# Performance work log

Hardware: AMD Instinct MI355X
Metric: run time of the kernel (lower is better)

The kernel has to match this reference:

```python
import jax, jax.numpy as jnp
import numpy as np

B, T, C, H = 2, 2048, 1024, 16
HD = C // H  # 64
EPS = 1e-5


def _layernorm(x, g, b):
    mu = jnp.mean(x, axis=-1, keepdims=True)
    var = jnp.mean(jnp.square(x - mu), axis=-1, keepdims=True)
    return (x - mu) * jax.lax.rsqrt(var + EPS) * g + b


def setup_inputs() -> dict:
    key = jax.random.key(0)
    ks = jax.random.split(key, 12)
    s = 0.02
    return {
        "x": jax.random.normal(ks[0], (B, T, C), dtype=jnp.float32),
        # per-head q/k/v projections stacked over heads: [H, C, HD]
        "Wq": jax.random.normal(ks[1], (H, C, HD), dtype=jnp.float32) * s,
        "Wk": jax.random.normal(ks[2], (H, C, HD), dtype=jnp.float32) * s,
        "Wv": jax.random.normal(ks[3], (H, C, HD), dtype=jnp.float32) * s,
        "Wp": jax.random.normal(ks[4], (C, C), dtype=jnp.float32) * s,
        "bp": jnp.zeros((C,), dtype=jnp.float32),
        "W1": jax.random.normal(ks[5], (C, 4 * C), dtype=jnp.float32) * s,
        "b1": jnp.zeros((4 * C,), dtype=jnp.float32),
        "W2": jax.random.normal(ks[6], (4 * C, C), dtype=jnp.float32) * s,
        "b2": jnp.zeros((C,), dtype=jnp.float32),
        "g1": jnp.ones((C,), dtype=jnp.float32),
        "be1": jnp.zeros((C,), dtype=jnp.float32),
        "g2": jnp.ones((C,), dtype=jnp.float32),
        "be2": jnp.zeros((C,), dtype=jnp.float32),
    }


def reference(x, Wq, Wk, Wv, Wp, bp, W1, b1, W2, b2, g1, be1, g2, be2):
    b, t, c = x.shape
    hd = Wq.shape[-1]
    # multi-head causal self-attention (heads vectorized instead of Python loop)
    q = jnp.einsum('btc,hcd->bhtd', x, Wq)
    k = jnp.einsum('btc,hcd->bhtd', x, Wk)
    v = jnp.einsum('btc,hcd->bhtd', x, Wv)
    scores = jnp.einsum('bhtd,bhsd->bhts', q, k) * (float(hd) ** -0.5)
    causal = jnp.tril(jnp.ones((t, t), dtype=bool))
    scores = jnp.where(causal, scores, -jnp.inf)
    probs = jax.nn.softmax(scores, axis=-1)  # dropout is identity in eval
    o = jnp.einsum('bhts,bhsd->bhtd', probs, v)
    o = o.transpose(0, 2, 1, 3).reshape(b, t, c)  # concat heads
    attn_out = o @ Wp + bp
    # residual + post-norm
    x = _layernorm(x + attn_out, g1, be1)
    # FFN (dropout identity in eval)
    ff = jax.nn.relu(x @ W1 + b1) @ W2 + b2
    x = _layernorm(x + ff, g2, be2)
    return x
```

## Files before the change

kernel.cpp:

```cpp
#include <hip/hip_runtime.h>
#include <cstdint>
#include <cstddef>

typedef __attribute__((ext_vector_type(8))) short short8;
typedef __attribute__((ext_vector_type(4))) short short4v;
typedef __attribute__((ext_vector_type(4))) float f32x4;
typedef __attribute__((ext_vector_type(2))) uint32_t u32x2;

#define Bdim 2
#define Tdim 2048
#define Cdim 1024
#define Hdim 16
#define HDdim 64
#define Mdim (Bdim*Tdim)
#define FFdim (4*Cdim)

__device__ __forceinline__ uint16_t f2bf(float f) {
    union { float f; uint32_t u; } v; v.f = f;
    uint32_t x = v.u;
    uint32_t r = x + 0x7FFFu + ((x >> 16) & 1u);
    return (uint16_t)(r >> 16);
}
__device__ __forceinline__ float bf2f(uint16_t h) {
    union { float f; uint32_t u; } v; v.u = ((uint32_t)h) << 16; return v.f;
}
__device__ __forceinline__ uint32_t cvtpk(float lo, float hi) {
    uint32_t r;
    asm("v_cvt_pk_bf16_f32 %0, %1, %2" : "=v"(r) : "v"(lo), "v"(hi));
    return r;
}

__device__ __forceinline__ void gload_lds16(const uint16_t* g, uint16_t* l) {
    __builtin_amdgcn_global_load_lds(
        (const __attribute__((address_space(1))) void*)g,
        (__attribute__((address_space(3))) void*)l, 16, 0, 0);
}

#define RAW_BAR()   asm volatile("s_barrier" ::: "memory")
#define VMCNT(N)    asm volatile("s_waitcnt vmcnt(" #N ")" ::: "memory")
#define LGKM0()     asm volatile("s_waitcnt lgkmcnt(0)" ::: "memory")

__global__ __launch_bounds__(256) void cast4_k(const float* __restrict__ in,
                                               uint16_t* __restrict__ out) {
    int i = (blockIdx.x * 256 + threadIdx.x) * 4;
    f32x4 v = *(const f32x4*)(in + i);
    short4v o;
#pragma unroll
    for (int j = 0; j < 4; ++j) o[j] = (short)f2bf(v[j]);
    *(short4v*)(out + i) = o;
}

__global__ __launch_bounds__(256) void transpose_tile(const float* __restrict__ in,
                                                      uint16_t* __restrict__ out,
                                                      int R, int Cc,
                                                      size_t ibs, size_t obs) {
    __shared__ uint16_t tile[32][33];
    const float* ip = in + (size_t)blockIdx.z * ibs;
    uint16_t* op = out + (size_t)blockIdx.z * obs;
    int r0 = blockIdx.x * 32, n0 = blockIdx.y * 32;
    int tx = threadIdx.x, ty = threadIdx.y;
#pragma unroll
    for (int i = 0; i < 4; ++i) {
        int r = ty + 8 * i;
        tile[r][tx] = f2bf(ip[(size_t)(r0 + r) * Cc + n0 + tx]);
    }
    __syncthreads();
#pragma unroll
    for (int i = 0; i < 4; ++i) {
        int n = ty + 8 * i;
        op[(size_t)(n0 + n) * R + r0 + tx] = tile[tx][n];
    }
}

__global__ __launch_bounds__(256) void vtrans_k(const uint16_t* __restrict__ qkv,
                                                uint16_t* __restrict__ vT) {
    __shared__ uint16_t tile[32][33];
    const int bh = blockIdx.z, b = bh >> 4, h = bh & 15;
    const uint16_t* vp = qkv + (size_t)b * Tdim * (3 * Cdim) + 2 * Cdim + h * HDdim;
    uint16_t* op = vT + (size_t)bh * HDdim * Tdim;
    const int t0 = blockIdx.x * 32, d0 = blockIdx.y * 32;
    const int tx = threadIdx.x, ty = threadIdx.y;
#pragma unroll
    for (int i = 0; i < 4; ++i) {
        int r = ty + 8 * i;
        tile[r][tx] = vp[(size_t)(t0 + r) * (3 * Cdim) + d0 + tx];
    }
    __syncthreads();
    const int tp = t0 + (((tx >> 2) & 3) << 3) + (((tx >> 4) & 1) << 2) + (tx & 3);
#pragma unroll
    for (int i = 0; i < 4; ++i) {
        int d = ty + 8 * i;
        op[(size_t)(d0 + d) * Tdim + tp] = tile[tx][d];
    }
}

template<bool BIAS, bool RELU, bool RESID, bool OUTF>
__global__ __launch_bounds__(512, 4) void gemm128_k(const uint16_t* __restrict__ A,
                                                    const uint16_t* __restrict__ Bt,
                                                    int Kfull, int Kp,
                                                    float* outF,
                                                    uint16_t* __restrict__ outB,
                                                    const float* __restrict__ bias,
                                                    const float* resid,
                                                    uint16_t* __restrict__ outP1,
                                                    uint16_t* __restrict__ outP2,
                                                    uint16_t* __restrict__ outP3,
                                                    int N) {
    __shared__ uint16_t lds[32768];
    const int bx = blockIdx.x, by = blockIdx.y, kz = blockIdx.z;
    const int tid = threadIdx.x;
    const int wave = tid >> 6, lane = tid & 63;
    const int lg = lane >> 4, lr = lane & 15, lr7 = lr & 7;
    const int wm = wave >> 2, wn = wave & 3;
    const int NT = Kp >> 6;

    const int aOff = wm * 4096 + lr * 64;
    const int bOff = 16384 + wn * 2048 + lr * 64;
    const int g0 = 8 * (lg ^ lr7);
    const int g1 = 8 * ((4 + lg) ^ lr7);

    const int srow = tid >> 3;
    const int scol = 8 * ((tid & 7) ^ (srow & 7));
    const uint16_t* aSrc = A + (size_t)(bx * 128 + srow) * Kfull + (size_t)kz * Kp + scol;
    const uint16_t* bSrc = Bt + (size_t)(by * 128 + srow) * Kfull + (size_t)kz * Kp + scol;
    const size_t r64 = (size_t)64 * Kfull;

#define STG_A(pp, tt) do {                                                        \
        _Pragma("unroll")                                                         \
        for (int h_ = 0; h_ < 2; ++h_)                                            \
            gload_lds16(aSrc + h_ * r64 + (size_t)(tt) * 64,                      \
                        &lds[(pp) * 8192 + h_ * 4096 + wave * 512]);              \
    } while (0)
#define STG_B(pp, tt) do {                                                        \
        _Pragma("unroll")                                                         \
        for (int h_ = 0; h_ < 2; ++h_)                                            \
            gload_lds16(bSrc + h_ * r64 + (size_t)(tt) * 64,                      \
                        &lds[16384 + (pp) * 8192 + h_ * 4096 + wave * 512]);      \
    } while (0)
#define MM(M, Nn, AF, BF) acc[M][Nn] = __builtin_amdgcn_mfma_f32_16x16x32_bf16(AF, BF, acc[M][Nn], 0, 0, 0)

    f32x4 acc[4][2];
#pragma unroll
    for (int i = 0; i < 4; ++i)
#pragma unroll
        for (int j = 0; j < 2; ++j) acc[i][j] = (f32x4){0.f, 0.f, 0.f, 0.f};

    STG_B(0, 0); STG_A(0, 0);
    if (NT > 1) { STG_B(1, 1); STG_A(1, 1); VMCNT(4); }
    else VMCNT(0);
    RAW_BAR();

    for (int t = 0; t < NT; ++t) {
        const int p = t & 1, p13 = p << 13;
        const bool nx1 = (t + 1 < NT), nx2 = (t + 2 < NT);
        short8 a0[4], b0[2], a1[4], b1[2];

#pragma unroll
        for (int m = 0; m < 4; ++m) a0[m] = *(const short8*)&lds[p13 + aOff + 1024 * m + g0];
#pragma unroll
        for (int nn = 0; nn < 2; ++nn) b0[nn] = *(const short8*)&lds[p13 + bOff + 1024 * nn + g0];
        __builtin_amdgcn_s_setprio(1);
#pragma unroll
        for (int m = 0; m < 4; ++m)
#pragma unroll
            for (int nn = 0; nn < 2; ++nn) MM(m, nn, a0[m], b0[nn]);
        __builtin_amdgcn_s_setprio(0);

#pragma unroll
        for (int m = 0; m < 4; ++m) a1[m] = *(const short8*)&lds[p13 + aOff + 1024 * m + g1];
#pragma unroll
        for (int nn = 0; nn < 2; ++nn) b1[nn] = *(const short8*)&lds[p13 + bOff + 1024 * nn + g1];
        __builtin_amdgcn_s_setprio(1);
#pragma unroll
        for (int m = 0; m < 4; ++m)
#pragma unroll
            for (int nn = 0; nn < 2; ++nn) MM(m, nn, a1[m], b1[nn]);
        __builtin_amdgcn_s_setprio(0);

        LGKM0();
        RAW_BAR();
        if (nx2) { STG_B(p, t + 2); STG_A(p, t + 2); }
        if (nx1) {
            if (nx2) VMCNT(4); else VMCNT(0);
            RAW_BAR();
        }
    }
#undef STG_A
#undef STG_B
#undef MM
    if (kz == 0) {
#pragma unroll
        for (int nn = 0; nn < 2; ++nn) {
            const int col = (by << 7) + wn * 32 + 16 * nn + lr;
            const float bv = BIAS ? bias[col] : 0.f;
#pragma unroll
            for (int m = 0; m < 4; ++m) {
#pragma unroll
                for (int r = 0; r < 4; ++r) {
                    const int row = (bx << 7) + wm * 64 + 16 * m + 4 * lg + r;
                    float v = acc[m][nn][r] + bv;
                    if (RELU) v = fmaxf(v, 0.f);
                    if (RESID) v += resid[(size_t)row * N + col];
                    if (OUTF) outF[(size_t)row * N + col] = v;
                    else      outB[(size_t)row * N + col] = f2bf(v);
                }
            }
        }
    } else {
        uint16_t* op = (kz == 1) ? outP1 : (kz == 2) ? outP2 : outP3;
#pragma unroll
        for (int nn = 0; nn < 2; ++nn) {
            const int col = (by << 7) + wn * 32 + 16 * nn + lr;
#pragma unroll
            for (int m = 0; m < 4; ++m) {
#pragma unroll
                for (int r = 0; r < 4; ++r) {
                    const int row = (bx << 7) + wm * 64 + 16 * m + 4 * lg + r;
                    op[(size_t)row * N + col] = f2bf(acc[m][nn][r]);
                }
            }
        }
    }
}

__global__ __launch_bounds__(256) void attn_k(const uint16_t* __restrict__ qkv,
                                              const uint16_t* __restrict__ vT,
                                              uint16_t* __restrict__ o) {
    __shared__ uint16_t Kb[2][64 * 64];
    __shared__ uint16_t Vb[2][64 * 64];
    const int tid = threadIdx.x;
    const int wave = tid >> 6, lane = tid & 63;
    const int lg = lane >> 4, lr = lane & 15, lr7 = lr & 7;
    const int bh = blockIdx.x, b = bh >> 4, h = bh & 15;
    const size_t rs = 3 * Cdim;
    const uint16_t* qp = qkv + (size_t)b * Tdim * rs + (size_t)h * HDdim;
    const uint16_t* kp = qp + Cdim;
    const uint16_t* vtp = vT + (size_t)bh * HDdim * Tdim;

    const int s0 = tid, s1 = tid + 256;
    const int r0v = s0 >> 3, c0v = ((s0 & 7) ^ (r0v & 7)) << 3;
    const int r1v = s1 >> 3, c1v = ((s1 & 7) ^ (r1v & 7)) << 3;
    const int db0 = wave * 512, db1 = 2048 + wave * 512;

#define STAGE(bufi, kvb)                                                        \
    do {                                                                        \
        gload_lds16(kp + (size_t)((kvb) + r0v) * rs + c0v, &Kb[bufi][db0]);     \
        gload_lds16(kp + (size_t)((kvb) + r1v) * rs + c1v, &Kb[bufi][db1]);     \
        gload_lds16(vtp + (size_t)r0v * Tdim + (kvb) + c0v, &Vb[bufi][db0]);    \
        gload_lds16(vtp + (size_t)r1v * Tdim + (kvb) + c1v, &Vb[bufi][db1]);    \
    } while (0)

    const int tiles[2] = {(int)blockIdx.y, 31 - (int)blockIdx.y};

    for (int ti = 0; ti < 2; ++ti) {
        const int tx = tiles[ti];
        const int q0 = tx << 6;
        const int nch = tx + 1;
        const int qrow = q0 + 16 * wave + lr;

        short8 qf[2];
#pragma unroll
        for (int c = 0; c < 2; ++c) {
            short8 raw = *(const short8*)(qp + (size_t)qrow * rs + 32 * c + 8 * lg);
#pragma unroll
            for (int j = 0; j < 8; ++j)
                qf[c][j] = (short)f2bf(bf2f((uint16_t)raw[j]) * 0.125f);
        }

        float m_run = -__builtin_inff(), l_run = 0.f;
        f32x4 oacc[4];
#pragma unroll
        for (int t = 0; t < 4; ++t) oacc[t] = (f32x4){0.f, 0.f, 0.f, 0.f};

        STAGE(0, 0);
        __syncthreads();
        int cur = 0;
        for (int ch = 0; ch < nch; ++ch) {
            if (ch + 1 < nch) STAGE(cur ^ 1, 64 * (ch + 1));
            const int kvb = 64 * ch;
            const char* Kc = (const char*)&Kb[cur][0];
            const char* Vc = (const char*)&Vb[cur][0];
            short8 kf[4][2];
#pragma unroll
            for (int u = 0; u < 4; ++u)
#pragma unroll
                for (int c = 0; c < 2; ++c)
                    kf[u][c] = *(const short8*)(Kc + (16 * u + lr) * 128 +
                                                (((lg + 4 * c) ^ lr7) << 4));
            f32x4 s4[4];
            __builtin_amdgcn_s_setprio(1);
#pragma unroll
            for (int u = 0; u < 4; ++u) {
                f32x4 z = (f32x4){0.f, 0.f, 0.f, 0.f};
                z = __builtin_amdgcn_mfma_f32_16x16x32_bf16(kf[u][0], qf[0], z, 0, 0, 0);
                z = __builtin_amdgcn_mfma_f32_16x16x32_bf16(kf[u][1], qf[1], z, 0, 0, 0);
                s4[u] = z;
            }
            __builtin_amdgcn_s_setprio(0);
            float p[4][4];
            float mx;
            if (ch + 1 == nch) {
                mx = -__builtin_inff();
#pragma unroll
                for (int u = 0; u < 4; ++u)
#pragma unroll
                    for (int r = 0; r < 4; ++r) {
                        int kv = kvb + 16 * u + 4 * lg + r;
                        float sv = (kv <= qrow) ? s4[u][r] : -__builtin_inff();
                        p[u][r] = sv;
                        mx = fmaxf(mx, sv);
                    }
            } else {
#pragma unroll
                for (int u = 0; u < 4; ++u)
#pragma unroll
                    for (int r = 0; r < 4; ++r) p[u][r] = s4[u][r];
                f32x4 m4;
#pragma unroll
                for (int r = 0; r < 4; ++r)
                    m4[r] = fmaxf(fmaxf(s4[0][r], s4[1][r]), fmaxf(s4[2][r], s4[3][r]));
                mx = fmaxf(fmaxf(m4[0], m4[1]), fmaxf(m4[2], m4[3]));
            }
            mx = fmaxf(mx, __shfl_xor(mx, 16));
            mx = fmaxf(mx, __shfl_xor(mx, 32));
            if (!__all(mx <= m_run + 8.f)) {
                const float m_new = fmaxf(m_run, mx);
                const float alpha = __expf(m_run - m_new);
#pragma unroll
                for (int t = 0; t < 4; ++t)
#pragma unroll
                    for (int r = 0; r < 4; ++r) oacc[t][r] *= alpha;
                l_run *= alpha;
                m_run = m_new;
            }
            float ps = 0.f;
#pragma unroll
            for (int u = 0; u < 4; ++u)
#pragma unroll
                for (int r = 0; r < 4; ++r) {
                    float e = __expf(p[u][r] - m_run);
                    p[u][r] = e; ps += e;
                }
            ps += __shfl_xor(ps, 16);
            ps += __shfl_xor(ps, 32);
            l_run += ps;
            short8 pb[2];
#pragma unroll
            for (int hh = 0; hh < 2; ++hh) {
                union { uint32_t w[4]; short8 v; } q_;
                q_.w[0] = cvtpk(p[2 * hh][0], p[2 * hh][1]);
                q_.w[1] = cvtpk(p[2 * hh][2], p[2 * hh][3]);
                q_.w[2] = cvtpk(p[2 * hh + 1][0], p[2 * hh + 1][1]);
                q_.w[3] = cvtpk(p[2 * hh + 1][2], p[2 * hh + 1][3]);
                pb[hh] = q_.v;
            }
            __builtin_amdgcn_s_setprio(1);
#pragma unroll
            for (int t = 0; t < 4; ++t) {
                const int vbase = (16 * t + lr) * 128;
                f32x4 oa = oacc[t];
#pragma unroll
                for (int hh = 0; hh < 2; ++hh) {
                    short8 vf = *(const short8*)(Vc + vbase + (((4 * hh + lg) ^ lr7) << 4));
                    oa = __builtin_amdgcn_mfma_f32_16x16x32_bf16(vf, pb[hh], oa, 0, 0, 0);
                }
                oacc[t] = oa;
            }
            __builtin_amdgcn_s_setprio(0);
            __syncthreads();
            cur ^= 1;
        }
        const float inv = 1.f / l_run;
        uint16_t* orow = o + (size_t)(b * Tdim + qrow) * Cdim + h * HDdim;
#pragma unroll
        for (int t = 0; t < 4; ++t) {
            u32x2 wv;
            wv[0] = cvtpk(oacc[t][0] * inv, oacc[t][1] * inv);
            wv[1] = cvtpk(oacc[t][2] * inv, oacc[t][3] * inv);
            *(u32x2*)(orow + 16 * t + 4 * lg) = wv;
        }
        __syncthreads();
    }
#undef STAGE
}

__global__ __launch_bounds__(256) void ln_k(const float* __restrict__ in,
                                            const uint16_t* __restrict__ in2b,
                                            const float* __restrict__ g,
                                            const float* __restrict__ be,
                                            float* __restrict__ outF,
                                            uint16_t* __restrict__ outB) {
    const int row = blockIdx.x, tid = threadIdx.x;
    const size_t base = (size_t)row * Cdim + tid * 4;
    f32x4 xv = *(const f32x4*)(in + base);
    if (in2b) {
        short4v yv = *(const short4v*)(in2b + base);
#pragma unroll
        for (int j = 0; j < 4; ++j) xv[j] += bf2f((uint16_t)yv[j]);
    }
    float s = xv[0] + xv[1] + xv[2] + xv[3];
    float q = xv[0] * xv[0] + xv[1] * xv[1] + xv[2] * xv[2] + xv[3] * xv[3];
#pragma unroll
    for (int off = 1; off < 64; off <<= 1) { s += __shfl_xor(s, off); q += __shfl_xor(q, off); }
    __shared__ float sm[4], sq[4];
    if ((tid & 63) == 0) { sm[tid >> 6] = s; sq[tid >> 6] = q; }
    __syncthreads();
    s = sm[0] + sm[1] + sm[2] + sm[3];
    q = sq[0] + sq[1] + sq[2] + sq[3];
    const float mu = s * (1.f / 1024.f);
    const float var = q * (1.f / 1024.f) - mu * mu;
    const float rstd = rsqrtf(var + 1e-5f);
#pragma unroll
    for (int j = 0; j < 4; ++j) {
        int col = tid * 4 + j;
        float y = (xv[j] - mu) * rstd * g[col] + be[col];
        if (outF) outF[(size_t)row * Cdim + col] = y;
        if (outB) outB[(size_t)row * Cdim + col] = f2bf(y);
    }
}

__global__ __launch_bounds__(256) void lnp_k(const float* __restrict__ in,
                                             const uint16_t* __restrict__ p2,
                                             const uint16_t* __restrict__ p3,
                                             const uint16_t* __restrict__ p4,
                                             const float* __restrict__ g,
                                             const float* __restrict__ be,
                                             float* __restrict__ outF) {
    const int row = blockIdx.x, tid = threadIdx.x;
    const size_t base = (size_t)row * Cdim + tid * 4;
    f32x4 xv = *(const f32x4*)(in + base);
    short4v a2 = *(const short4v*)(p2 + base);
    short4v a3 = *(const short4v*)(p3 + base);
    short4v a4 = *(const short4v*)(p4 + base);
#pragma unroll
    for (int j = 0; j < 4; ++j)
        xv[j] += bf2f((uint16_t)a2[j]) + bf2f((uint16_t)a3[j]) + bf2f((uint16_t)a4[j]);
    float s = xv[0] + xv[1] + xv[2] + xv[3];
    float q = xv[0] * xv[0] + xv[1] * xv[1] + xv[2] * xv[2] + xv[3] * xv[3];
#pragma unroll
    for (int off = 1; off < 64; off <<= 1) { s += __shfl_xor(s, off); q += __shfl_xor(q, off); }
    __shared__ float sm[4], sq[4];
    if ((tid & 63) == 0) { sm[tid >> 6] = s; sq[tid >> 6] = q; }
    __syncthreads();
    s = sm[0] + sm[1] + sm[2] + sm[3];
    q = sq[0] + sq[1] + sq[2] + sq[3];
    const float mu = s * (1.f / 1024.f);
    const float var = q * (1.f / 1024.f) - mu * mu;
    const float rstd = rsqrtf(var + 1e-5f);
#pragma unroll
    for (int j = 0; j < 4; ++j) {
        int col = tid * 4 + j;
        outF[(size_t)row * Cdim + col] = (xv[j] - mu) * rstd * g[col] + be[col];
    }
}

extern "C" void kernel_launch(void* const* d_in, const int* in_sizes, int n_in,
                              void* d_out, int out_size, void* d_ws, size_t ws_size,
                              hipStream_t stream) {
    const float* x   = (const float*)d_in[0];
    const float* Wq  = (const float*)d_in[1];
    const float* Wk  = (const float*)d_in[2];
    const float* Wv  = (const float*)d_in[3];
    const float* Wp  = (const float*)d_in[4];
    const float* bp  = (const float*)d_in[5];
    const float* W1  = (const float*)d_in[6];
    const float* b1  = (const float*)d_in[7];
    const float* W2  = (const float*)d_in[8];
    const float* b2  = (const float*)d_in[9];
    const float* g1  = (const float*)d_in[10];
    const float* be1 = (const float*)d_in[11];
    const float* g2  = (const float*)d_in[12];
    const float* be2 = (const float*)d_in[13];
    float* out = (float*)d_out;

    char* ws = (char*)d_ws;
    uint16_t* qkv   = (uint16_t*)(ws + 0);
    uint16_t* P1p   = (uint16_t*)(ws + 0);
    uint16_t* h1    = (uint16_t*)(ws + 0);
    uint16_t* obuf  = (uint16_t*)(ws + 25165824);
    uint16_t* xb    = (uint16_t*)(ws + 33554432);
    uint16_t* vT    = (uint16_t*)(ws + 33554432);
    uint16_t* x1b   = (uint16_t*)(ws + 33554432);
    uint16_t* Q2    = (uint16_t*)(ws + 33554432);
    uint16_t* wqkv  = (uint16_t*)(ws + 41943040);
    uint16_t* wpt   = (uint16_t*)(ws + 48234496);
    float*    resid = (float*)   (ws + 50331648);
    uint16_t* Q1    = (uint16_t*)(ws + 50331648);
    float*    x1f   = (float*)   (ws + 67108864);
    uint16_t* w1t   = (uint16_t*)(ws + 83886080);
    uint16_t* w2t   = (uint16_t*)(ws + 92274688);
    uint16_t* Q3    = (uint16_t*)(ws + 100663296);

    cast4_k<<<4096, 256, 0, stream>>>(x, xb);
    transpose_tile<<<dim3(32, 2, 16), dim3(32, 8), 0, stream>>>(Wq, wqkv,           1024, 64, 65536, 65536);
    transpose_tile<<<dim3(32, 2, 16), dim3(32, 8), 0, stream>>>(Wk, wqkv + 1048576, 1024, 64, 65536, 65536);
    transpose_tile<<<dim3(32, 2, 16), dim3(32, 8), 0, stream>>>(Wv, wqkv + 2097152, 1024, 64, 65536, 65536);
    transpose_tile<<<dim3(32, 32, 1),  dim3(32, 8), 0, stream>>>(Wp, wpt, 1024, 1024, 0, 0);
    transpose_tile<<<dim3(32, 128, 1), dim3(32, 8), 0, stream>>>(W1, w1t, 1024, 4096, 0, 0);
    transpose_tile<<<dim3(128, 32, 1), dim3(32, 8), 0, stream>>>(W2, w2t, 4096, 1024, 0, 0);

    gemm128_k<false, false, false, false><<<dim3(32, 24, 1), 512, 0, stream>>>(
        xb, wqkv, Cdim, Cdim, nullptr, qkv, nullptr, nullptr,
        nullptr, nullptr, nullptr, 3 * Cdim);
    vtrans_k<<<dim3(64, 2, 32), dim3(32, 8), 0, stream>>>(qkv, vT);
    attn_k<<<dim3(32, 16), 256, 0, stream>>>(qkv, vT, obuf);
    gemm128_k<true, false, true, true><<<dim3(32, 8, 2), 512, 0, stream>>>(
        obuf, wpt, Cdim, Cdim / 2, resid, nullptr, bp, x,
        P1p, nullptr, nullptr, Cdim);
    ln_k<<<Mdim, 256, 0, stream>>>(resid, P1p, g1, be1, x1f, x1b);
    gemm128_k<true, true, false, false><<<dim3(32, 32, 1), 512, 0, stream>>>(
        x1b, w1t, Cdim, Cdim, nullptr, h1, b1, nullptr,
        nullptr, nullptr, nullptr, FFdim);
    gemm128_k<true, false, true, true><<<dim3(32, 8, 4), 512, 0, stream>>>(
        h1, w2t, FFdim, FFdim / 4, x1f, nullptr, b2, x1f,
        Q1, Q2, Q3, Cdim);
    lnp_k<<<Mdim, 256, 0, stream>>>(x1f, Q1, Q2, Q3, g2, be2, out);
}
```

Baseline: 244.5 us.

## Split attention into one query tile per block with exp2 softmax and lane-local sums

The attention kernel now runs one query tile per block on a 32x32 grid, instead of each block processing a paired short/long tile. Tiles are ordered in interleaved groups so heavy and light causal tiles mix across the grid. The softmax folds log2(e) into the Q scale so it can use exp2f, and it keeps row sums per lane, reducing them across lanes once at the end. The max reduction is skipped when no lane exceeds the threshold, which is raised to 11.5 in the log2 domain. This doubles the block count and removes per-chunk shuffles, at the cost of relying on the hardware scheduler for load balance.

```diff
diff --git a/kernel.cpp b/kernel.cpp
--- a/kernel.cpp
+++ b/kernel.cpp
@@ -232,6 +232,8 @@
     const int wave = tid >> 6, lane = tid & 63;
     const int lg = lane >> 4, lr = lane & 15, lr7 = lr & 7;
     const int bh = blockIdx.x, b = bh >> 4, h = bh & 15;
+    const int yy = blockIdx.y, k4 = yy >> 3, y0 = yy & 7;
+    const int tx = (k4 == 0) ? y0 : (k4 == 1) ? 31 - y0 : (k4 == 2) ? 8 + y0 : 23 - y0;
     const size_t rs = 3 * Cdim;
     const uint16_t* qp = qkv + (size_t)b * Tdim * rs + (size_t)h * HDdim;
     const uint16_t* kp = qp + Cdim;
@@ -250,136 +252,129 @@
         gload_lds16(vtp + (size_t)r1v * Tdim + (kvb) + c1v, &Vb[bufi][db1]);    \
     } while (0)
 
-    const int tiles[2] = {(int)blockIdx.y, 31 - (int)blockIdx.y};
-
-    for (int ti = 0; ti < 2; ++ti) {
-        const int tx = tiles[ti];
-        const int q0 = tx << 6;
-        const int nch = tx + 1;
-        const int qrow = q0 + 16 * wave + lr;
-
-        short8 qf[2];
-#pragma unroll
-        for (int c = 0; c < 2; ++c) {
-            short8 raw = *(const short8*)(qp + (size_t)qrow * rs + 32 * c + 8 * lg);
-#pragma unroll
-            for (int j = 0; j < 8; ++j)
-                qf[c][j] = (short)f2bf(bf2f((uint16_t)raw[j]) * 0.125f);
-        }
-
-        float m_run = -__builtin_inff(), l_run = 0.f;
-        f32x4 oacc[4];
-#pragma unroll
-        for (int t = 0; t < 4; ++t) oacc[t] = (f32x4){0.f, 0.f, 0.f, 0.f};
-
-        STAGE(0, 0);
+    const int q0 = tx << 6;
+    const int nch = tx + 1;
+    const int qrow = q0 + 16 * wave + lr;
+
+    short8 qf[2];
+#pragma unroll
+    for (int c = 0; c < 2; ++c) {
+        short8 raw = *(const short8*)(qp + (size_t)qrow * rs + 32 * c + 8 * lg);
+#pragma unroll
+        for (int j = 0; j < 8; ++j)
+            qf[c][j] = (short)f2bf(bf2f((uint16_t)raw[j]) * 0.18033688f);
+    }
+
+    float m_run = -__builtin_inff(), l_lane = 0.f;
+    f32x4 oacc[4];
+#pragma unroll
+    for (int t = 0; t < 4; ++t) oacc[t] = (f32x4){0.f, 0.f, 0.f, 0.f};
+
+    STAGE(0, 0);
+    __syncthreads();
+    int cur = 0;
+    for (int ch = 0; ch < nch; ++ch) {
+        if (ch + 1 < nch) STAGE(cur ^ 1, 64 * (ch + 1));
+        const int kvb = 64 * ch;
+        const char* Kc = (const char*)&Kb[cur][0];
+        const char* Vc = (const char*)&Vb[cur][0];
+        short8 kf[4][2];
+#pragma unroll
+        for (int u = 0; u < 4; ++u)
+#pragma unroll
+            for (int c = 0; c < 2; ++c)
+                kf[u][c] = *(const short8*)(Kc + (16 * u + lr) * 128 +
+                                            (((lg + 4 * c) ^ lr7) << 4));
+        f32x4 s4[4];
+        __builtin_amdgcn_s_setprio(1);
+#pragma unroll
+        for (int u = 0; u < 4; ++u) {
+            f32x4 z = (f32x4){0.f, 0.f, 0.f, 0.f};
+            z = __builtin_amdgcn_mfma_f32_16x16x32_bf16(kf[u][0], qf[0], z, 0, 0, 0);
+            z = __builtin_amdgcn_mfma_f32_16x16x32_bf16(kf[u][1], qf[1], z, 0, 0, 0);
+            s4[u] = z;
+        }
+        __builtin_amdgcn_s_setprio(0);
+        float p[4][4];
+        float mxl;
+        if (ch + 1 == nch) {
+            mxl = -__builtin_inff();
+#pragma unroll
+            for (int u = 0; u < 4; ++u)
+#pragma unroll
+                for (int r = 0; r < 4; ++r) {
+                    int kv = kvb + 16 * u + 4 * lg + r;
+                    float sv = (kv <= qrow) ? s4[u][r] : -__builtin_inff();
+                    p[u][r] = sv;
+                    mxl = fmaxf(mxl, sv);
+                }
+        } else {
+#pragma unroll
+            for (int u = 0; u < 4; ++u)
+#pragma unroll
+                for (int r = 0; r < 4; ++r) p[u][r] = s4[u][r];
+            f32x4 m4;
+#pragma unroll
+            for (int r = 0; r < 4; ++r)
+                m4[r] = fmaxf(fmaxf(s4[0][r], s4[1][r]), fmaxf(s4[2][r], s4[3][r]));
+            mxl = fmaxf(fmaxf(m4[0], m4[1]), fmaxf(m4[2], m4[3]));
+        }
+        if (!__all(mxl <= m_run + 11.5f)) {
+            float mx = fmaxf(mxl, __shfl_xor(mxl, 16));
+            mx = fmaxf(mx, __shfl_xor(mx, 32));
+            const float m_new = fmaxf(m_run, mx);
+            const float alpha = exp2f(m_run - m_new);
+#pragma unroll
+            for (int t = 0; t < 4; ++t)
+#pragma unroll
+                for (int r = 0; r < 4; ++r) oacc[t][r] *= alpha;
+            l_lane *= alpha;
+            m_run = m_new;
+        }
+#pragma unroll
+        for (int u = 0; u < 4; ++u)
+#pragma unroll
+            for (int r = 0; r < 4; ++r) {
+                float e = exp2f(p[u][r] - m_run);
+                p[u][r] = e; l_lane += e;
+            }
+        short8 pb[2];
+#pragma unroll
+        for (int hh = 0; hh < 2; ++hh) {
+            union { uint32_t w[4]; short8 v; } q_;
+            q_.w[0] = cvtpk(p[2 * hh][0], p[2 * hh][1]);
+            q_.w[1] = cvtpk(p[2 * hh][2], p[2 * hh][3]);
+            q_.w[2] = cvtpk(p[2 * hh + 1][0], p[2 * hh + 1][1]);
+            q_.w[3] = cvtpk(p[2 * hh + 1][2], p[2 * hh + 1][3]);
+            pb[hh] = q_.v;
+        }
+        __builtin_amdgcn_s_setprio(1);
+#pragma unroll
+        for (int t = 0; t < 4; ++t) {
+            const int vbase = (16 * t + lr) * 128;
+            f32x4 oa = oacc[t];
+#pragma unroll
+            for (int hh = 0; hh < 2; ++hh) {
+                short8 vf = *(const short8*)(Vc + vbase + (((4 * hh + lg) ^ lr7) << 4));
+                oa = __builtin_amdgcn_mfma_f32_16x16x32_bf16(vf, pb[hh], oa, 0, 0, 0);
+            }
+            oacc[t] = oa;
+        }
+        __builtin_amdgcn_s_setprio(0);
         __syncthreads();
-        int cur = 0;
-        for (int ch = 0; ch < nch; ++ch) {
-            if (ch + 1 < nch) STAGE(cur ^ 1, 64 * (ch + 1));
-            const int kvb = 64 * ch;
-            const char* Kc = (const char*)&Kb[cur][0];
-            const char* Vc = (const char*)&Vb[cur][0];
-            short8 kf[4][2];
-#pragma unroll
-            for (int u = 0; u < 4; ++u)
-#pragma unroll
-                for (int c = 0; c < 2; ++c)
-                    kf[u][c] = *(const short8*)(Kc + (16 * u + lr) * 128 +
-                                                (((lg + 4 * c) ^ lr7) << 4));
-            f32x4 s4[4];
-            __builtin_amdgcn_s_setprio(1);
-#pragma unroll
-            for (int u = 0; u < 4; ++u) {
-                f32x4 z = (f32x4){0.f, 0.f, 0.f, 0.f};
-                z = __builtin_amdgcn_mfma_f32_16x16x32_bf16(kf[u][0], qf[0], z, 0, 0, 0);
-                z = __builtin_amdgcn_mfma_f32_16x16x32_bf16(kf[u][1], qf[1], z, 0, 0, 0);
-                s4[u] = z;
-            }
-            __builtin_amdgcn_s_setprio(0);
-            float p[4][4];
-            float mx;
-            if (ch + 1 == nch) {
-                mx = -__builtin_inff();
-#pragma unroll
-                for (int u = 0; u < 4; ++u)
-#pragma unroll
-                    for (int r = 0; r < 4; ++r) {
-                        int kv = kvb + 16 * u + 4 * lg + r;
-                        float sv = (kv <= qrow) ? s4[u][r] : -__builtin_inff();
-                        p[u][r] = sv;
-                        mx = fmaxf(mx, sv);
-                    }
-            } else {
-#pragma unroll
-                for (int u = 0; u < 4; ++u)
-#pragma unroll
-                    for (int r = 0; r < 4; ++r) p[u][r] = s4[u][r];
-                f32x4 m4;
-#pragma unroll
-                for (int r = 0; r < 4; ++r)
-                    m4[r] = fmaxf(fmaxf(s4[0][r], s4[1][r]), fmaxf(s4[2][r], s4[3][r]));
-                mx = fmaxf(fmaxf(m4[0], m4[1]), fmaxf(m4[2], m4[3]));
-            }
-            mx = fmaxf(mx, __shfl_xor(mx, 16));
-            mx = fmaxf(mx, __shfl_xor(mx, 32));
-            if (!__all(mx <= m_run + 8.f)) {
-                const float m_new = fmaxf(m_run, mx);
-                const float alpha = __expf(m_run - m_new);
-#pragma unroll
-                for (int t = 0; t < 4; ++t)
-#pragma unroll
-                    for (int r = 0; r < 4; ++r) oacc[t][r] *= alpha;
-                l_run *= alpha;
-                m_run = m_new;
-            }
-            float ps = 0.f;
-#pragma unroll
-            for (int u = 0; u < 4; ++u)
-#pragma unroll
-                for (int r = 0; r < 4; ++r) {
-                    float e = __expf(p[u][r] - m_run);
-                    p[u][r] = e; ps += e;
-                }
-            ps += __shfl_xor(ps, 16);
-            ps += __shfl_xor(ps, 32);
-            l_run += ps;
-            short8 pb[2];
-#pragma unroll
-            for (int hh = 0; hh < 2; ++hh) {
-                union { uint32_t w[4]; short8 v; } q_;
-                q_.w[0] = cvtpk(p[2 * hh][0], p[2 * hh][1]);
-                q_.w[1] = cvtpk(p[2 * hh][2], p[2 * hh][3]);
-                q_.w[2] = cvtpk(p[2 * hh + 1][0], p[2 * hh + 1][1]);
-                q_.w[3] = cvtpk(p[2 * hh + 1][2], p[2 * hh + 1][3]);
-                pb[hh] = q_.v;
-            }
-            __builtin_amdgcn_s_setprio(1);
-#pragma unroll
-            for (int t = 0; t < 4; ++t) {
-                const int vbase = (16 * t + lr) * 128;
-                f32x4 oa = oacc[t];
-#pragma unroll
-                for (int hh = 0; hh < 2; ++hh) {
-                    short8 vf = *(const short8*)(Vc + vbase + (((4 * hh + lg) ^ lr7) << 4));
-                    oa = __builtin_amdgcn_mfma_f32_16x16x32_bf16(vf, pb[hh], oa, 0, 0, 0);
-                }
-                oacc[t] = oa;
-            }
-            __builtin_amdgcn_s_setprio(0);
-            __syncthreads();
-            cur ^= 1;
-        }
-        const float inv = 1.f / l_run;
-        uint16_t* orow = o + (size_t)(b * Tdim + qrow) * Cdim + h * HDdim;
-#pragma unroll
-        for (int t = 0; t < 4; ++t) {
-            u32x2 wv;
-            wv[0] = cvtpk(oacc[t][0] * inv, oacc[t][1] * inv);
-            wv[1] = cvtpk(oacc[t][2] * inv, oacc[t][3] * inv);
-            *(u32x2*)(orow + 16 * t + 4 * lg) = wv;
-        }
-        __syncthreads();
+        cur ^= 1;
+    }
+    float l = l_lane;
+    l += __shfl_xor(l, 16);
+    l += __shfl_xor(l, 32);
+    const float inv = 1.f / l;
+    uint16_t* orow = o + (size_t)(b * Tdim + qrow) * Cdim + h * HDdim;
+#pragma unroll
+    for (int t = 0; t < 4; ++t) {
+        u32x2 wv;
+        wv[0] = cvtpk(oacc[t][0] * inv, oacc[t][1] * inv);
+        wv[1] = cvtpk(oacc[t][2] * inv, oacc[t][3] * inv);
+        *(u32x2*)(orow + 16 * t + 4 * lg) = wv;
     }
 #undef STAGE
 }
@@ -503,7 +498,7 @@
         xb, wqkv, Cdim, Cdim, nullptr, qkv, nullptr, nullptr,
         nullptr, nullptr, nullptr, 3 * Cdim);
     vtrans_k<<<dim3(64, 2, 32), dim3(32, 8), 0, stream>>>(qkv, vT);
-    attn_k<<<dim3(32, 16), 256, 0, stream>>>(qkv, vT, obuf);
+    attn_k<<<dim3(32, 32), 256, 0, stream>>>(qkv, vT, obuf);
     gemm128_k<true, false, true, true><<<dim3(32, 8, 2), 512, 0, stream>>>(
         obuf, wpt, Cdim, Cdim / 2, resid, nullptr, bp, x,
         P1p, nullptr, nullptr, Cdim);
```

Result: no change. 242.9 us (-0.6%).
